# Kernel tuning notes

Hardware: AMD Instinct MI355X
Metric: run time of the kernel (lower is better)

The kernel has to match this reference:

```python
import jax, jax.numpy as jnp
import numpy as np

B, S, E, H = 4, 2048, 512, 8


def setup_inputs() -> dict:
    key = jax.random.key(0)
    ks = jax.random.split(key, 12)
    wsc = 1.0 / np.sqrt(E)  # torch Linear default uniform(-1/sqrt(in), 1/sqrt(in))
    u = lambda k, shape, s: jax.random.uniform(k, shape, jnp.float32, -s, s)
    return {
        "q": jax.random.normal(ks[0], (B, S, E), jnp.float32),
        "k": jax.random.normal(ks[1], (B, S, E), jnp.float32),
        "v": jax.random.normal(ks[2], (B, S, E), jnp.float32),
        # stacked per-head weights, torch layout [out, in] -> [H, E, E]
        "Wq": u(ks[3], (H, E, E), wsc), "bq": u(ks[4], (H, E), wsc),
        "Wk": u(ks[5], (H, E, E), wsc), "bk": u(ks[6], (H, E), wsc),
        "Wv": u(ks[7], (H, E, E), wsc), "bv": u(ks[8], (H, E), wsc),
        "Wo": u(ks[9], (E, H * E), 1.0 / np.sqrt(H * E)),
        "bo": u(ks[10], (E,), 1.0 / np.sqrt(H * E)),
    }


def reference(q, k, v, Wq, bq, Wk, bk, Wv, bv, Wo, bo):
    b, s, e = q.shape
    # per-head projections (torch Linear: y = x W^T + b), vectorized over heads
    qh = jnp.einsum('bse,hoe->bhso', q, Wq) + bq[None, :, None, :]  # [B,H,S,E]
    kh = jnp.einsum('bse,hoe->bhso', k, Wk) + bk[None, :, None, :]
    vh = jnp.einsum('bse,hoe->bhso', v, Wv) + bv[None, :, None, :]
    # NO softmax (faithful to source): (Q K^T) V / embed_dim
    scores = jnp.einsum('bhqe,bhke->bhqk', qh, kh)          # [B,H,S,S]
    out = jnp.einsum('bhqk,bhke->bhqe', scores, vh) / e     # [B,H,S,E]
    # concat heads along feature dim (head order preserved), then w_o
    out = out.transpose(0, 2, 1, 3).reshape(b, s, -1)        # [B,S,H*E]
    return jnp.einsum('bsf,of->bso', out, Wo) + bo
```

## Files before the change

kernel.cpp:

```cpp
#include <hip/hip_runtime.h>


typedef long long i64;
typedef unsigned short u16;
typedef __attribute__((ext_vector_type(8))) short bf16x8;
typedef __attribute__((ext_vector_type(4))) float f32x4;

#define EB 512
#define EP 640
#define SQ 2048
#define NB 4
#define NH 8
#define HEP 5120

#define OFF_KT    0ll
#define OFF_VT    10485760ll
#define OFF_WQT   20971520ll
#define OFF_WKT   26214400ll
#define OFF_WVT   31457280ll
#define OFF_WOB   36700160ll
#define OFF_ZCAT  40894464ll
#define OFF_UCAT  46137344ll
#define OFF_GP    52690944ll
#define OFF_GB    65798144ll
#define OFF_ZGC   0ll
#define OFF_CTP   20971520ll
#define OFF_QB    0ll
#define OFF_CTB   46137344ll
#define OFF_RB    48758784ll

__device__ __forceinline__ u16 f2bf(float x) {
    unsigned u = __float_as_uint(x);
    return (u16)((u + 0x7fffu + ((u >> 16) & 1u)) >> 16);
}

__device__ __forceinline__ void gload16(const void* g, void* l) {
    __builtin_amdgcn_global_load_lds(
        (const __attribute__((address_space(1))) unsigned int*)g,
        (__attribute__((address_space(3))) unsigned int*)l, 16, 0, 0);
}

__device__ __forceinline__ void gemm_body(
    const u16* __restrict__ A, i64 lda, const u16* __restrict__ B, i64 ldb,
    int bx, int by, int K, int epi, void* Cv, i64 ldc,
    const float* rbias, const float* bo, char* pool)
{
    char* lA0 = pool;
    char* lA1 = pool + 16384;
    char* lB0 = pool + 32768;
    char* lB1 = pool + 49152;
    const i64 m0 = (i64)bx * 128, n0 = (i64)by * 128;
    const int tid = threadIdx.x, lane = tid & 63, wid = tid >> 6;
    const int wr = wid >> 1, wc = wid & 1;
    const int g = lane >> 4, li = lane & 15;

    i64 offA[4], offB[4]; int lofs[4];
#pragma unroll
    for (int i = 0; i < 4; ++i) {
        const int chunk = i * 4 + wid;
        const int rr = chunk * 8 + (lane >> 3);
        const int gc = ((lane & 7) ^ (rr & 7)) << 3;
        offA[i] = (m0 + rr) * lda + gc;
        offB[i] = (n0 + rr) * ldb + gc;
        lofs[i] = chunk * 1024;
    }
    const int ldest = lane * 16;

    f32x4 acc[4][4];
#pragma unroll
    for (int a_ = 0; a_ < 4; ++a_)
#pragma unroll
        for (int b_ = 0; b_ < 4; ++b_) acc[a_][b_] = (f32x4){0.f, 0.f, 0.f, 0.f};

    char* bufA[2] = {lA0, lA1};
    char* bufB[2] = {lB0, lB1};
    const int nIt = K >> 6;

#pragma unroll
    for (int i = 0; i < 4; ++i) {
        gload16(A + offA[i], bufA[0] + lofs[i] + ldest);
        gload16(B + offB[i], bufB[0] + lofs[i] + ldest);
    }
    __syncthreads();

    int cur = 0;
    for (int it = 0; it < nIt; ++it) {
        if (it + 1 < nIt) {
            const i64 k0 = (i64)(it + 1) << 6;
#pragma unroll
            for (int i = 0; i < 4; ++i) {
                gload16(A + offA[i] + k0, bufA[cur ^ 1] + lofs[i] + ldest);
                gload16(B + offB[i] + k0, bufB[cur ^ 1] + lofs[i] + ldest);
            }
        }
        char* cA = bufA[cur];
        char* cB = bufB[cur];
#pragma unroll
        for (int ks = 0; ks < 2; ++ks) {
            bf16x8 af[4], bfr[4];
#pragma unroll
            for (int f = 0; f < 4; ++f) {
                const int row = wr * 64 + f * 16 + li;
                const int slot = (ks * 4 + g) ^ (row & 7);
                af[f] = *(const bf16x8*)(cA + row * 128 + slot * 16);
            }
#pragma unroll
            for (int f = 0; f < 4; ++f) {
                const int row = wc * 64 + f * 16 + li;
                const int slot = (ks * 4 + g) ^ (row & 7);
                bfr[f] = *(const bf16x8*)(cB + row * 128 + slot * 16);
            }
#pragma unroll
            for (int fm = 0; fm < 4; ++fm)
#pragma unroll
                for (int fn = 0; fn < 4; ++fn)
                    acc[fm][fn] = __builtin_amdgcn_mfma_f32_16x16x32_bf16(
                        af[fm], bfr[fn], acc[fm][fn], 0, 0, 0);
        }
        __syncthreads();
        cur ^= 1;
    }

    if (epi == 0) {
        u16* C = (u16*)Cv;
#pragma unroll
        for (int fm = 0; fm < 4; ++fm)
#pragma unroll
            for (int fn = 0; fn < 4; ++fn) {
                const i64 col = n0 + wc * 64 + fn * 16 + li;
#pragma unroll
                for (int q = 0; q < 4; ++q) {
                    const i64 row = m0 + wr * 64 + fm * 16 + g * 4 + q;
                    C[row * ldc + col] = f2bf(acc[fm][fn][q]);
                }
            }
    } else if (epi == 2) {
        float* C = (float*)Cv;
#pragma unroll
        for (int fn = 0; fn < 4; ++fn) {
            const i64 col = n0 + wc * 64 + fn * 16 + li;
            const float bb = rbias[col] + bo[col];
#pragma unroll
            for (int fm = 0; fm < 4; ++fm)
#pragma unroll
                for (int q = 0; q < 4; ++q) {
                    const i64 row = m0 + wr * 64 + fm * 16 + g * 4 + q;
                    C[row * ldc + col] = acc[fm][fn][q] + bb;
                }
        }
    } else {
        float* C = (float*)Cv;
#pragma unroll
        for (int fm = 0; fm < 4; ++fm)
#pragma unroll
            for (int fn = 0; fn < 4; ++fn)
                *(f32x4*)(C + (fm * 4 + fn) * 1024 + tid * 4) = acc[fm][fn];
    }
}

#define GEMM_LDS __shared__ __align__(16) char pool[65536];

__device__ __forceinline__ void transpose_dev(
    const float* __restrict__ src, const float* __restrict__ aug,
    u16* __restrict__ dst, int S, int bx, int by, char* pool)
{
    const int s0 = bx * 64, e0 = by * 64;
    const int t = threadIdx.x;
    if (e0 >= EB) {
#pragma unroll
        for (int i = 0; i < 16; ++i) {
            const int idx = i * 256 + t;
            const int er = idx >> 6, sc = idx & 63;
            const int e = e0 + er;
            u16 val = 0;
            if (e == EB) val = f2bf(aug ? aug[s0 + sc] : 1.0f);
            dst[(i64)e * S + s0 + sc] = val;
        }
        return;
    }
    float (*tile)[65] = (float(*)[65])pool;
#pragma unroll
    for (int i = 0; i < 16; ++i) {
        const int idx = i * 256 + t;
        const int sr = idx >> 6, ec = idx & 63;
        tile[sr][ec] = src[(i64)(s0 + sr) * EB + e0 + ec];
    }
    __syncthreads();
#pragma unroll
    for (int i = 0; i < 16; ++i) {
        const int idx = i * 256 + t;
        const int er = idx >> 6, sc = idx & 63;
        dst[(i64)(e0 + er) * S + s0 + sc] = f2bf(tile[sc][er]);
    }
}

__device__ __forceinline__ void cvt_dev(const float4* in, ushort4* outp,
                                        float alpha, i64 i)
{
    const float4 v = in[i];
    ushort4 o;
    o.x = f2bf(v.x * alpha); o.y = f2bf(v.y * alpha);
    o.z = f2bf(v.z * alpha); o.w = f2bf(v.w * alpha);
    outp[i] = o;
}

__global__ __launch_bounds__(256)
void prep(const float* __restrict__ k, const float* __restrict__ v,
          const float* __restrict__ Wq, const float* __restrict__ bq,
          const float* __restrict__ Wk, const float* __restrict__ bk,
          const float* __restrict__ Wv, const float* __restrict__ bv,
          const float* __restrict__ Wo, char* __restrict__ ws)
{
    __shared__ __align__(16) char pool[16640];
    const int u = blockIdx.x, t = threadIdx.x;
    if (u < 1280) {
        const int bz = u / 320, r = u % 320;
        transpose_dev(k + (i64)bz * SQ * EB, nullptr,
                      (u16*)(ws + OFF_KT) + (i64)bz * EP * SQ, SQ,
                      r % 32, r / 32, pool);
    } else if (u < 2560) {
        const int l = u - 1280, bz = l / 320, r = l % 320;
        transpose_dev(v + (i64)bz * SQ * EB, nullptr,
                      (u16*)(ws + OFF_VT) + (i64)bz * EP * SQ, SQ,
                      r % 32, r / 32, pool);
    } else if (u < 3200) {
        const int l = u - 2560, bz = l / 80, r = l % 80;
        transpose_dev(Wq + (i64)bz * EB * EB, bq + (i64)bz * EB,
                      (u16*)(ws + OFF_WQT) + (i64)bz * EP * EB, EB,
                      r % 8, r / 8, pool);
    } else if (u < 3840) {
        const int l = u - 3200, bz = l / 80, r = l % 80;
        transpose_dev(Wk + (i64)bz * EB * EB, bk + (i64)bz * EB,
                      (u16*)(ws + OFF_WKT) + (i64)bz * EP * EB, EB,
                      r % 8, r / 8, pool);
    } else if (u < 4480) {
        const int l = u - 3840, bz = l / 80, r = l % 80;
        transpose_dev(Wv + (i64)bz * EB * EB, bv + (i64)bz * EB,
                      (u16*)(ws + OFF_WVT) + (i64)bz * EP * EB, EB,
                      r % 8, r / 8, pool);
    } else {
        const i64 j = u - 4480;
#pragma unroll
        for (int s = 0; s < 4; ++s)
            cvt_dev((const float4*)Wo, (ushort4*)(ws + OFF_WOB), 1.0f,
                    j * 1024 + s * 256 + t);
    }
}

__global__ __launch_bounds__(256)
void stage1(char* __restrict__ ws)
{
    GEMM_LDS
    const int x = blockIdx.x & 7, o = blockIdx.x >> 3;
    if (o < 25) {
        const int gu = x * 25 + o;
        const int b = gu / 50, sp = (gu % 50) / 25, r = gu % 25;
        const u16* A = (const u16*)(ws + OFF_KT) + (i64)b * EP * SQ + sp * 1024;
        const u16* B = (const u16*)(ws + OFF_VT) + (i64)b * EP * SQ + sp * 1024;
        float* C = (float*)(ws + OFF_GP) + ((i64)(b * 2 + sp) * 25 + r) * 16384;
        gemm_body(A, SQ, B, SQ, r / 5, r % 5, 1024, 3, C, 0, nullptr, nullptr, pool);
    } else {
        const int j = x * 45 + (o - 25);
        if (j < 200) {
            const int h = j / 25, r = j % 25;
            gemm_body((const u16*)(ws + OFF_WQT) + (i64)h * EP * EB, EB,
                      (const u16*)(ws + OFF_WKT) + (i64)h * EP * EB, EB,
                      r / 5, r % 5, EB, 0,
                      (u16*)(ws + OFF_UCAT) + (i64)h * EP, HEP,
                      nullptr, nullptr, pool);
        } else {
            const int j2 = j - 200, h = j2 / 20, r = j2 % 20;
            gemm_body((const u16*)(ws + OFF_WOB) + (i64)h * EB, (i64)NH * EB,
                      (const u16*)(ws + OFF_WVT) + (i64)h * EP * EB, EB,
                      r / 5, r % 5, EB, 0,
                      (u16*)(ws + OFF_ZCAT) + (i64)h * EP, HEP,
                      nullptr, nullptr, pool);
        }
    }
}

__global__ __launch_bounds__(256)
void gred(char* __restrict__ ws)
{
    const int u = blockIdx.x;
    const int b = u / 25, t = u % 25;
    const int bx = t / 5, by = t % 5;
    const int tid = threadIdx.x, lane = tid & 63, wid = tid >> 6;
    const int wr = wid >> 1, wc = wid & 1, g = lane >> 4, li = lane & 15;
    const float* base = (const float*)(ws + OFF_GP) + ((i64)b * 2 * 25 + t) * 16384;
    u16* gb = (u16*)(ws + OFF_GB) + (i64)b * EP * EP;
#pragma unroll
    for (int fm = 0; fm < 4; ++fm)
#pragma unroll
        for (int fn = 0; fn < 4; ++fn) {
            const int fo = (fm * 4 + fn) * 1024 + tid * 4;
            f32x4 s = *(const f32x4*)(base + fo);
            f32x4 p1 = *(const f32x4*)(base + 25 * 16384 + fo);
            s[0] += p1[0]; s[1] += p1[1]; s[2] += p1[2]; s[3] += p1[3];
            const int row0 = bx * 128 + wr * 64 + fm * 16 + g * 4;
            const int col = by * 128 + wc * 64 + fn * 16 + li;
#pragma unroll
            for (int qq = 0; qq < 4; ++qq)
                gb[(i64)(row0 + qq) * EP + col] = f2bf(s[qq]);
        }
}

__global__ __launch_bounds__(256)
void zg(char* __restrict__ ws)
{
    GEMM_LDS
    const int x = blockIdx.x & 7, o = blockIdx.x >> 3;
    const int id = x * 80 + o;
    const int z = id / 20, t = id % 20, b = z >> 3, h = z & 7;
    gemm_body((const u16*)(ws + OFF_ZCAT) + (i64)h * EP, HEP,
              (const u16*)(ws + OFF_GB) + (i64)b * EP * EP, EP,
              t / 5, t % 5, EP, 0,
              (u16*)(ws + OFF_ZGC) + (i64)b * EB * HEP + (i64)h * EP, HEP,
              nullptr, nullptr, pool);
}

__global__ __launch_bounds__(256)
void ct(char* __restrict__ ws)
{
    GEMM_LDS
    const int x = blockIdx.x & 7, o = blockIdx.x >> 3;
    const int id = x * 40 + o;
    const int z = id / 20, t = id % 20, b = z >> 2, sp = z & 3;
    const u16* A = (const u16*)(ws + OFF_ZGC) + (i64)b * EB * HEP + (i64)sp * 1280;
    const u16* B = (const u16*)(ws + OFF_UCAT) + (i64)sp * 1280;
    float* C = (float*)(ws + OFF_CTP) + ((i64)(b * 4 + sp) * 20 + t) * 16384;
    gemm_body(A, HEP, B, HEP, t / 5, t % 5, 1280, 3, C, 0,
              nullptr, nullptr, pool);
}

__global__ __launch_bounds__(256)
void cvt2(char* __restrict__ ws, const float* __restrict__ q)
{
    const int u = blockIdx.x, tid = threadIdx.x;
    if (u < 80) {
        const int b = u / 20, t = u % 20;
        const int bx = t / 5, by = t % 5;
        const int lane = tid & 63, wid = tid >> 6;
        const int wr = wid >> 1, wc = wid & 1, g = lane >> 4, li = lane & 15;
        const float* base = (const float*)(ws + OFF_CTP) + ((i64)b * 4 * 20 + t) * 16384;
        u16* ctb = (u16*)(ws + OFF_CTB) + (i64)b * EB * EP;
        float* rb = (float*)(ws + OFF_RB) + (i64)b * EB;
#pragma unroll
        for (int fm = 0; fm < 4; ++fm)
#pragma unroll
            for (int fn = 0; fn < 4; ++fn) {
                const int fo = (fm * 4 + fn) * 1024 + tid * 4;
                f32x4 s = *(const f32x4*)(base + fo);
#pragma unroll
                for (int p = 1; p < 4; ++p) {
                    f32x4 pp = *(const f32x4*)(base + (i64)p * 20 * 16384 + fo);
                    s[0] += pp[0]; s[1] += pp[1]; s[2] += pp[2]; s[3] += pp[3];
                }
                const int row0 = bx * 128 + wr * 64 + fm * 16 + g * 4;
                const int col = by * 128 + wc * 64 + fn * 16 + li;
#pragma unroll
                for (int qq = 0; qq < 4; ++qq) {
                    const float val = s[qq] * (1.0f / 512.0f);
                    ctb[(i64)(row0 + qq) * EP + col] = f2bf(val);
                    if (col == 512) rb[row0 + qq] = val;
                }
            }
    } else {
        const i64 j = u - 80;
#pragma unroll
        for (int s = 0; s < 4; ++s)
            cvt_dev((const float4*)q, (ushort4*)(ws + OFF_QB), 1.0f,
                    j * 1024 + s * 256 + tid);
    }
}

__global__ __launch_bounds__(256)
void gout(char* __restrict__ ws, float* __restrict__ out,
          const float* __restrict__ bo)
{
    GEMM_LDS
    const int x = blockIdx.x & 7, o = blockIdx.x >> 3;
    const int id = x * 32 + o;
    const int b = id / 64, t = id % 64;
    gemm_body((const u16*)(ws + OFF_QB) + (i64)b * SQ * EB, EB,
              (const u16*)(ws + OFF_CTB) + (i64)b * EB * EP, EP,
              t / 4, t % 4, EB, 2,
              out + (i64)b * SQ * EB, EB,
              (const float*)(ws + OFF_RB) + (i64)b * EB, bo, pool);
}

extern "C" void kernel_launch(void* const* d_in, const int* in_sizes, int n_in,
                              void* d_out, int out_size, void* d_ws, size_t ws_size,
                              hipStream_t stream)
{
    const float* q  = (const float*)d_in[0];
    const float* k  = (const float*)d_in[1];
    const float* v  = (const float*)d_in[2];
    const float* Wq = (const float*)d_in[3];
    const float* bq = (const float*)d_in[4];
    const float* Wk = (const float*)d_in[5];
    const float* bk = (const float*)d_in[6];
    const float* Wv = (const float*)d_in[7];
    const float* bv = (const float*)d_in[8];
    const float* Wo = (const float*)d_in[9];
    const float* bo = (const float*)d_in[10];
    float* out = (float*)d_out;
    char* ws = (char*)d_ws;
    (void)in_sizes; (void)n_in; (void)out_size; (void)ws_size;

    const dim3 blk(256);

    prep<<<dim3(4992), blk, 0, stream>>>(k, v, Wq, bq, Wk, bk, Wv, bv, Wo, ws);
    stage1<<<dim3(560), blk, 0, stream>>>(ws);
    gred<<<dim3(100), blk, 0, stream>>>(ws);
    zg<<<dim3(640), blk, 0, stream>>>(ws);
    ct<<<dim3(320), blk, 0, stream>>>(ws);
    cvt2<<<dim3(1104), blk, 0, stream>>>(ws, q);
    gout<<<dim3(256), blk, 0, stream>>>(ws, out, bo);
}
```

Baseline: 264.2 us.

## Shrink GEMM tiles to 64x128 and drop LDS double buffering for more blocks

New measurement: 223.0 us. 15.6% less time.

```diff
diff --git a/kernel.cpp b/kernel.cpp
--- a/kernel.cpp
+++ b/kernel.cpp
@@ -40,85 +40,64 @@
         (__attribute__((address_space(3))) unsigned int*)l, 16, 0, 0);
 }
 
-__device__ __forceinline__ void gemm_body(
+__device__ __forceinline__ void gemm64(
     const u16* __restrict__ A, i64 lda, const u16* __restrict__ B, i64 ldb,
     int bx, int by, int K, int epi, void* Cv, i64 ldc,
     const float* rbias, const float* bo, char* pool)
 {
-    char* lA0 = pool;
-    char* lA1 = pool + 16384;
-    char* lB0 = pool + 32768;
-    char* lB1 = pool + 49152;
-    const i64 m0 = (i64)bx * 128, n0 = (i64)by * 128;
+    char* lA = pool;
+    char* lB = pool + 8192;
+    const i64 m0 = (i64)bx * 64, n0 = (i64)by * 128;
     const int tid = threadIdx.x, lane = tid & 63, wid = tid >> 6;
-    const int wr = wid >> 1, wc = wid & 1;
     const int g = lane >> 4, li = lane & 15;
 
-    i64 offA[4], offB[4]; int lofs[4];
-#pragma unroll
-    for (int i = 0; i < 4; ++i) {
-        const int chunk = i * 4 + wid;
-        const int rr = chunk * 8 + (lane >> 3);
+    const u16* gsrc[6]; char* ldst[6];
+#pragma unroll
+    for (int i = 0; i < 6; ++i) {
+        const int c = wid * 6 + i;
+        const bool isA = c < 8;
+        const int cc = isA ? c : c - 8;
+        const int rr = cc * 8 + (lane >> 3);
         const int gc = ((lane & 7) ^ (rr & 7)) << 3;
-        offA[i] = (m0 + rr) * lda + gc;
-        offB[i] = (n0 + rr) * ldb + gc;
-        lofs[i] = chunk * 1024;
-    }
-    const int ldest = lane * 16;
-
-    f32x4 acc[4][4];
+        gsrc[i] = (isA ? A + (m0 + rr) * lda : B + (n0 + rr) * ldb) + gc;
+        ldst[i] = (isA ? lA + c * 1024 : lB + cc * 1024) + lane * 16;
+    }
+
+    f32x4 acc[4][2];
 #pragma unroll
     for (int a_ = 0; a_ < 4; ++a_)
 #pragma unroll
-        for (int b_ = 0; b_ < 4; ++b_) acc[a_][b_] = (f32x4){0.f, 0.f, 0.f, 0.f};
-
-    char* bufA[2] = {lA0, lA1};
-    char* bufB[2] = {lB0, lB1};
+        for (int b_ = 0; b_ < 2; ++b_) acc[a_][b_] = (f32x4){0.f, 0.f, 0.f, 0.f};
+
     const int nIt = K >> 6;
-
-#pragma unroll
-    for (int i = 0; i < 4; ++i) {
-        gload16(A + offA[i], bufA[0] + lofs[i] + ldest);
-        gload16(B + offB[i], bufB[0] + lofs[i] + ldest);
-    }
-    __syncthreads();
-
-    int cur = 0;
     for (int it = 0; it < nIt; ++it) {
-        if (it + 1 < nIt) {
-            const i64 k0 = (i64)(it + 1) << 6;
-#pragma unroll
-            for (int i = 0; i < 4; ++i) {
-                gload16(A + offA[i] + k0, bufA[cur ^ 1] + lofs[i] + ldest);
-                gload16(B + offB[i] + k0, bufB[cur ^ 1] + lofs[i] + ldest);
+        const i64 k0 = (i64)it << 6;
+#pragma unroll
+        for (int i = 0; i < 6; ++i) gload16(gsrc[i] + k0, ldst[i]);
+        __syncthreads();
+#pragma unroll
+        for (int ks = 0; ks < 2; ++ks) {
+            bf16x8 af[4], bf[2];
+#pragma unroll
+            for (int fm = 0; fm < 4; ++fm) {
+                const int row = fm * 16 + li;
+                const int slot = (ks * 4 + g) ^ (row & 7);
+                af[fm] = *(const bf16x8*)(lA + row * 128 + slot * 16);
             }
-        }
-        char* cA = bufA[cur];
-        char* cB = bufB[cur];
-#pragma unroll
-        for (int ks = 0; ks < 2; ++ks) {
-            bf16x8 af[4], bfr[4];
-#pragma unroll
-            for (int f = 0; f < 4; ++f) {
-                const int row = wr * 64 + f * 16 + li;
+#pragma unroll
+            for (int fn = 0; fn < 2; ++fn) {
+                const int row = wid * 32 + fn * 16 + li;
                 const int slot = (ks * 4 + g) ^ (row & 7);
-                af[f] = *(const bf16x8*)(cA + row * 128 + slot * 16);
+                bf[fn] = *(const bf16x8*)(lB + row * 128 + slot * 16);
             }
 #pragma unroll
-            for (int f = 0; f < 4; ++f) {
-                const int row = wc * 64 + f * 16 + li;
-                const int slot = (ks * 4 + g) ^ (row & 7);
-                bfr[f] = *(const bf16x8*)(cB + row * 128 + slot * 16);
-            }
-#pragma unroll
             for (int fm = 0; fm < 4; ++fm)
 #pragma unroll
-                for (int fn = 0; fn < 4; ++fn)
+                for (int fn = 0; fn < 2; ++fn)
                     acc[fm][fn] = __builtin_amdgcn_mfma_f32_16x16x32_bf16(
-                        af[fm], bfr[fn], acc[fm][fn], 0, 0, 0);
+                        af[fm], bf[fn], acc[fm][fn], 0, 0, 0);
         }
         __syncthreads();
-        cur ^= 1;
     }
 
     if (epi == 0) {
@@ -126,25 +105,25 @@
 #pragma unroll
         for (int fm = 0; fm < 4; ++fm)
 #pragma unroll
-            for (int fn = 0; fn < 4; ++fn) {
-                const i64 col = n0 + wc * 64 + fn * 16 + li;
+            for (int fn = 0; fn < 2; ++fn) {
+                const i64 col = n0 + wid * 32 + fn * 16 + li;
 #pragma unroll
                 for (int q = 0; q < 4; ++q) {
-                    const i64 row = m0 + wr * 64 + fm * 16 + g * 4 + q;
+                    const i64 row = m0 + fm * 16 + g * 4 + q;
                     C[row * ldc + col] = f2bf(acc[fm][fn][q]);
                 }
             }
     } else if (epi == 2) {
         float* C = (float*)Cv;
 #pragma unroll
-        for (int fn = 0; fn < 4; ++fn) {
-            const i64 col = n0 + wc * 64 + fn * 16 + li;
+        for (int fn = 0; fn < 2; ++fn) {
+            const i64 col = n0 + wid * 32 + fn * 16 + li;
             const float bb = rbias[col] + bo[col];
 #pragma unroll
             for (int fm = 0; fm < 4; ++fm)
 #pragma unroll
                 for (int q = 0; q < 4; ++q) {
-                    const i64 row = m0 + wr * 64 + fm * 16 + g * 4 + q;
+                    const i64 row = m0 + fm * 16 + g * 4 + q;
                     C[row * ldc + col] = acc[fm][fn][q] + bb;
                 }
         }
@@ -153,12 +132,12 @@
 #pragma unroll
         for (int fm = 0; fm < 4; ++fm)
 #pragma unroll
-            for (int fn = 0; fn < 4; ++fn)
-                *(f32x4*)(C + (fm * 4 + fn) * 1024 + tid * 4) = acc[fm][fn];
-    }
-}
-
-#define GEMM_LDS __shared__ __align__(16) char pool[65536];
+            for (int fn = 0; fn < 2; ++fn)
+                *(f32x4*)(C + (fm * 2 + fn) * 1024 + tid * 4) = acc[fm][fn];
+    }
+}
+
+#define GEMM_LDS __shared__ __align__(16) char pool[24576];
 
 __device__ __forceinline__ void transpose_dev(
     const float* __restrict__ src, const float* __restrict__ aug,
@@ -252,29 +231,29 @@
 {
     GEMM_LDS
     const int x = blockIdx.x & 7, o = blockIdx.x >> 3;
-    if (o < 25) {
-        const int gu = x * 25 + o;
-        const int b = gu / 50, sp = (gu % 50) / 25, r = gu % 25;
+    if (o < 50) {
+        const int gu = x * 50 + o;
+        const int b = gu / 100, sp = (gu / 50) & 1, r = gu % 50;
         const u16* A = (const u16*)(ws + OFF_KT) + (i64)b * EP * SQ + sp * 1024;
         const u16* B = (const u16*)(ws + OFF_VT) + (i64)b * EP * SQ + sp * 1024;
-        float* C = (float*)(ws + OFF_GP) + ((i64)(b * 2 + sp) * 25 + r) * 16384;
-        gemm_body(A, SQ, B, SQ, r / 5, r % 5, 1024, 3, C, 0, nullptr, nullptr, pool);
+        float* C = (float*)(ws + OFF_GP) + ((i64)(b * 2 + sp) * 50 + r) * 8192;
+        gemm64(A, SQ, B, SQ, r / 5, r % 5, 1024, 3, C, 0, nullptr, nullptr, pool);
     } else {
-        const int j = x * 45 + (o - 25);
-        if (j < 200) {
-            const int h = j / 25, r = j % 25;
-            gemm_body((const u16*)(ws + OFF_WQT) + (i64)h * EP * EB, EB,
-                      (const u16*)(ws + OFF_WKT) + (i64)h * EP * EB, EB,
-                      r / 5, r % 5, EB, 0,
-                      (u16*)(ws + OFF_UCAT) + (i64)h * EP, HEP,
-                      nullptr, nullptr, pool);
+        const int j = x * 90 + (o - 50);
+        if (j < 400) {
+            const int h = j / 50, r = j % 50;
+            gemm64((const u16*)(ws + OFF_WQT) + (i64)h * EP * EB, EB,
+                   (const u16*)(ws + OFF_WKT) + (i64)h * EP * EB, EB,
+                   r / 5, r % 5, EB, 0,
+                   (u16*)(ws + OFF_UCAT) + (i64)h * EP, HEP,
+                   nullptr, nullptr, pool);
         } else {
-            const int j2 = j - 200, h = j2 / 20, r = j2 % 20;
-            gemm_body((const u16*)(ws + OFF_WOB) + (i64)h * EB, (i64)NH * EB,
-                      (const u16*)(ws + OFF_WVT) + (i64)h * EP * EB, EB,
-                      r / 5, r % 5, EB, 0,
-                      (u16*)(ws + OFF_ZCAT) + (i64)h * EP, HEP,
-                      nullptr, nullptr, pool);
+            const int j2 = j - 400, h = j2 / 40, r = j2 % 40;
+            gemm64((const u16*)(ws + OFF_WOB) + (i64)h * EB, (i64)NH * EB,
+                   (const u16*)(ws + OFF_WVT) + (i64)h * EP * EB, EB,
+                   r / 5, r % 5, EB, 0,
+                   (u16*)(ws + OFF_ZCAT) + (i64)h * EP, HEP,
+                   nullptr, nullptr, pool);
         }
     }
 }
@@ -283,22 +262,22 @@
 void gred(char* __restrict__ ws)
 {
     const int u = blockIdx.x;
-    const int b = u / 25, t = u % 25;
+    const int b = u / 50, t = u % 50;
     const int bx = t / 5, by = t % 5;
     const int tid = threadIdx.x, lane = tid & 63, wid = tid >> 6;
-    const int wr = wid >> 1, wc = wid & 1, g = lane >> 4, li = lane & 15;
-    const float* base = (const float*)(ws + OFF_GP) + ((i64)b * 2 * 25 + t) * 16384;
+    const int g = lane >> 4, li = lane & 15;
+    const float* base = (const float*)(ws + OFF_GP) + ((i64)b * 2 * 50 + t) * 8192;
     u16* gb = (u16*)(ws + OFF_GB) + (i64)b * EP * EP;
 #pragma unroll
     for (int fm = 0; fm < 4; ++fm)
 #pragma unroll
-        for (int fn = 0; fn < 4; ++fn) {
-            const int fo = (fm * 4 + fn) * 1024 + tid * 4;
+        for (int fn = 0; fn < 2; ++fn) {
+            const int fo = (fm * 2 + fn) * 1024 + tid * 4;
             f32x4 s = *(const f32x4*)(base + fo);
-            f32x4 p1 = *(const f32x4*)(base + 25 * 16384 + fo);
+            f32x4 p1 = *(const f32x4*)(base + 50 * 8192 + fo);
             s[0] += p1[0]; s[1] += p1[1]; s[2] += p1[2]; s[3] += p1[3];
-            const int row0 = bx * 128 + wr * 64 + fm * 16 + g * 4;
-            const int col = by * 128 + wc * 64 + fn * 16 + li;
+            const int row0 = bx * 64 + fm * 16 + g * 4;
+            const int col = by * 128 + wid * 32 + fn * 16 + li;
 #pragma unroll
             for (int qq = 0; qq < 4; ++qq)
                 gb[(i64)(row0 + qq) * EP + col] = f2bf(s[qq]);
@@ -307,57 +286,57 @@
 
 __global__ __launch_bounds__(256)
 void zg(char* __restrict__ ws)
+{
+    GEMM_LDS
+    const int x = blockIdx.x & 7, o = blockIdx.x >> 3;
+    const int id = x * 160 + o;
+    const int z = id / 40, t = id % 40, b = z >> 3, h = z & 7;
+    gemm64((const u16*)(ws + OFF_ZCAT) + (i64)h * EP, HEP,
+           (const u16*)(ws + OFF_GB) + (i64)b * EP * EP, EP,
+           t / 5, t % 5, EP, 0,
+           (u16*)(ws + OFF_ZGC) + (i64)b * EB * HEP + (i64)h * EP, HEP,
+           nullptr, nullptr, pool);
+}
+
+__global__ __launch_bounds__(256)
+void ct(char* __restrict__ ws)
 {
     GEMM_LDS
     const int x = blockIdx.x & 7, o = blockIdx.x >> 3;
     const int id = x * 80 + o;
-    const int z = id / 20, t = id % 20, b = z >> 3, h = z & 7;
-    gemm_body((const u16*)(ws + OFF_ZCAT) + (i64)h * EP, HEP,
-              (const u16*)(ws + OFF_GB) + (i64)b * EP * EP, EP,
-              t / 5, t % 5, EP, 0,
-              (u16*)(ws + OFF_ZGC) + (i64)b * EB * HEP + (i64)h * EP, HEP,
-              nullptr, nullptr, pool);
-}
-
-__global__ __launch_bounds__(256)
-void ct(char* __restrict__ ws)
-{
-    GEMM_LDS
-    const int x = blockIdx.x & 7, o = blockIdx.x >> 3;
-    const int id = x * 40 + o;
-    const int z = id / 20, t = id % 20, b = z >> 2, sp = z & 3;
+    const int z = id / 40, t = id % 40, b = z >> 2, sp = z & 3;
     const u16* A = (const u16*)(ws + OFF_ZGC) + (i64)b * EB * HEP + (i64)sp * 1280;
     const u16* B = (const u16*)(ws + OFF_UCAT) + (i64)sp * 1280;
-    float* C = (float*)(ws + OFF_CTP) + ((i64)(b * 4 + sp) * 20 + t) * 16384;
-    gemm_body(A, HEP, B, HEP, t / 5, t % 5, 1280, 3, C, 0,
-              nullptr, nullptr, pool);
+    float* C = (float*)(ws + OFF_CTP) + ((i64)(b * 4 + sp) * 40 + t) * 8192;
+    gemm64(A, HEP, B, HEP, t / 5, t % 5, 1280, 3, C, 0,
+           nullptr, nullptr, pool);
 }
 
 __global__ __launch_bounds__(256)
 void cvt2(char* __restrict__ ws, const float* __restrict__ q)
 {
     const int u = blockIdx.x, tid = threadIdx.x;
-    if (u < 80) {
-        const int b = u / 20, t = u % 20;
+    if (u < 160) {
+        const int b = u / 40, t = u % 40;
         const int bx = t / 5, by = t % 5;
         const int lane = tid & 63, wid = tid >> 6;
-        const int wr = wid >> 1, wc = wid & 1, g = lane >> 4, li = lane & 15;
-        const float* base = (const float*)(ws + OFF_CTP) + ((i64)b * 4 * 20 + t) * 16384;
+        const int g = lane >> 4, li = lane & 15;
+        const float* base = (const float*)(ws + OFF_CTP) + ((i64)b * 4 * 40 + t) * 8192;
         u16* ctb = (u16*)(ws + OFF_CTB) + (i64)b * EB * EP;
         float* rb = (float*)(ws + OFF_RB) + (i64)b * EB;
 #pragma unroll
         for (int fm = 0; fm < 4; ++fm)
 #pragma unroll
-            for (int fn = 0; fn < 4; ++fn) {
-                const int fo = (fm * 4 + fn) * 1024 + tid * 4;
+            for (int fn = 0; fn < 2; ++fn) {
+                const int fo = (fm * 2 + fn) * 1024 + tid * 4;
                 f32x4 s = *(const f32x4*)(base + fo);
 #pragma unroll
                 for (int p = 1; p < 4; ++p) {
-                    f32x4 pp = *(const f32x4*)(base + (i64)p * 20 * 16384 + fo);
+                    f32x4 pp = *(const f32x4*)(base + (i64)p * 40 * 8192 + fo);
                     s[0] += pp[0]; s[1] += pp[1]; s[2] += pp[2]; s[3] += pp[3];
                 }
-                const int row0 = bx * 128 + wr * 64 + fm * 16 + g * 4;
-                const int col = by * 128 + wc * 64 + fn * 16 + li;
+                const int row0 = bx * 64 + fm * 16 + g * 4;
+                const int col = by * 128 + wid * 32 + fn * 16 + li;
 #pragma unroll
                 for (int qq = 0; qq < 4; ++qq) {
                     const float val = s[qq] * (1.0f / 512.0f);
@@ -366,11 +345,13 @@
                 }
             }
     } else {
-        const i64 j = u - 80;
-#pragma unroll
-        for (int s = 0; s < 4; ++s)
-            cvt_dev((const float4*)q, (ushort4*)(ws + OFF_QB), 1.0f,
-                    j * 1024 + s * 256 + tid);
+        const i64 j = u - 160;
+        if (j < 1024) {
+#pragma unroll
+            for (int s = 0; s < 4; ++s)
+                cvt_dev((const float4*)q, (ushort4*)(ws + OFF_QB), 1.0f,
+                        j * 1024 + s * 256 + tid);
+        }
     }
 }
 
@@ -380,13 +361,13 @@
 {
     GEMM_LDS
     const int x = blockIdx.x & 7, o = blockIdx.x >> 3;
-    const int id = x * 32 + o;
-    const int b = id / 64, t = id % 64;
-    gemm_body((const u16*)(ws + OFF_QB) + (i64)b * SQ * EB, EB,
-              (const u16*)(ws + OFF_CTB) + (i64)b * EB * EP, EP,
-              t / 4, t % 4, EB, 2,
-              out + (i64)b * SQ * EB, EB,
-              (const float*)(ws + OFF_RB) + (i64)b * EB, bo, pool);
+    const int id = x * 64 + o;
+    const int b = id / 128, t = id % 128;
+    gemm64((const u16*)(ws + OFF_QB) + (i64)b * SQ * EB, EB,
+           (const u16*)(ws + OFF_CTB) + (i64)b * EB * EP, EP,
+           t / 4, t % 4, EB, 2,
+           out + (i64)b * SQ * EB, EB,
+           (const float*)(ws + OFF_RB) + (i64)b * EB, bo, pool);
 }
 
 extern "C" void kernel_launch(void* const* d_in, const int* in_sizes, int n_in,
@@ -411,10 +392,10 @@
     const dim3 blk(256);
 
     prep<<<dim3(4992), blk, 0, stream>>>(k, v, Wq, bq, Wk, bk, Wv, bv, Wo, ws);
-    stage1<<<dim3(560), blk, 0, stream>>>(ws);
-    gred<<<dim3(100), blk, 0, stream>>>(ws);
-    zg<<<dim3(640), blk, 0, stream>>>(ws);
-    ct<<<dim3(320), blk, 0, stream>>>(ws);
-    cvt2<<<dim3(1104), blk, 0, stream>>>(ws, q);
-    gout<<<dim3(256), blk, 0, stream>>>(ws, out, bo);
-}
+    stage1<<<dim3(1120), blk, 0, stream>>>(ws);
+    gred<<<dim3(200), blk, 0, stream>>>(ws);
+    zg<<<dim3(1280), blk, 0, stream>>>(ws);
+    ct<<<dim3(640), blk, 0, stream>>>(ws);
+    cvt2<<<dim3(1184), blk, 0, stream>>>(ws, q);
+    gout<<<dim3(512), blk, 0, stream>>>(ws, out, bo);
+}
```
